# Kernel optimization log

Measured on AMD Instinct MI355X. Metric: run time of the kernel, lower is better.

## Reference

```python
import jax, jax.numpy as jnp
import numpy as np

N_HEADS = 8
N_POINTS = 4


def _grid_sample_bilinear(img, x, y):
    """PyTorch-style grid_sample, mode='bilinear', align_corners=True, zeros padding.
    img: [G, D, Hk, Wk]; x, y: [G, P] pixel coords. Returns [G, D, P]."""
    G, D, Hk, Wk = img.shape
    x0 = jnp.floor(x); y0 = jnp.floor(y)
    x1 = x0 + 1.0; y1 = y0 + 1.0
    wx1 = x - x0; wx0 = 1.0 - wx1
    wy1 = y - y0; wy0 = 1.0 - wy1
    imgf = img.reshape(G, D, Hk * Wk)

    def corner(xi, yi, w):
        valid = (xi >= 0) & (xi <= Wk - 1) & (yi >= 0) & (yi <= Hk - 1)
        ix = jnp.clip(xi, 0, Wk - 1).astype(jnp.int32)
        iy = jnp.clip(yi, 0, Hk - 1).astype(jnp.int32)
        idx = iy * Wk + ix  # [G, P]
        g = jax.vmap(lambda im, i: jnp.take(im, i, axis=1))(imgf, idx)  # [G, D, P]
        return g * (w * valid.astype(w.dtype))[:, None, :]

    return (corner(x0, y0, wx0 * wy0) + corner(x1, y0, wx1 * wy0)
            + corner(x0, y1, wx0 * wy1) + corner(x1, y1, wx1 * wy1))


def setup_inputs() -> dict:
    key = jax.random.key(0)
    ks = jax.random.split(key, 6)
    B, C, H, W = 8, 256, 64, 64
    return {
        "query": jax.random.normal(ks[0], (B, C, H, W), jnp.float32),
        "key": jax.random.normal(ks[1], (B, C, H, W), jnp.float32),
        "w_off": jax.random.normal(ks[2], (N_HEADS * N_POINTS * 3, C), jnp.float32) * 0.02,
        "b_off": jax.random.normal(ks[3], (N_HEADS * N_POINTS * 3,), jnp.float32) * 0.02,
        "w_proj": jax.random.normal(ks[4], (C, C), jnp.float32) * 0.02,
        "b_proj": jax.random.normal(ks[5], (C,), jnp.float32) * 0.02,
    }


def reference(query, key, w_off, b_off, w_proj, b_proj):
    B, C, H, W = query.shape
    Hk, Wk = key.shape[2], key.shape[3]
    d_head = C // N_HEADS

    # [B, N, C]
    q = query.reshape(B, C, H * W).transpose(0, 2, 1)
    ow = q @ w_off.T + b_off                      # [B, N, heads*points*3]
    ow = ow.reshape(B, H, W, N_HEADS, N_POINTS, 3)
    offsets = ow[..., :2]                          # [B,H,W,h,p,2]
    wts = jax.nn.softmax(ow[..., 2], axis=-1)      # [B,H,W,h,p]

    gy, gx = jnp.meshgrid(jnp.linspace(-1.0, 1.0, H, dtype=query.dtype),
                          jnp.linspace(-1.0, 1.0, W, dtype=query.dtype), indexing='ij')
    grid = jnp.stack([gx, gy], axis=-1).reshape(1, H, W, 1, 1, 2)
    locs = grid + offsets * 0.1                    # [B,H,W,h,p,2] normalized coords
    locs = locs.transpose(0, 3, 4, 1, 2, 5)        # [B,h,p,H,W,2]

    G = B * N_HEADS
    locs = locs.reshape(G, N_POINTS * H * W, 2)
    xg = (locs[..., 0] + 1.0) * 0.5 * (Wk - 1)     # align_corners=True mapping
    yg = (locs[..., 1] + 1.0) * 0.5 * (Hk - 1)

    key_r = key.reshape(G, d_head, Hk, Wk)
    sampled = _grid_sample_bilinear(key_r, xg, yg)            # [G, d_head, p*H*W]
    sampled = sampled.reshape(B, N_HEADS, d_head, N_POINTS, H, W)

    w = wts.transpose(0, 3, 4, 1, 2)               # [B,h,p,H,W]
    out_feat = jnp.einsum('bhdpxy,bhpxy->bhdxy', sampled, w)  # [B,h,d,H,W]
    out_feat = out_feat.reshape(B, C, H * W).transpose(0, 2, 1)  # [B,N,C]
    return out_feat @ w_proj.T + b_proj
```

## Files before the change

kernel.cpp:

```cpp
#include <hip/hip_runtime.h>
#include <hip/hip_fp16.h>
#include <cstdint>

#define B_   8
#define C_   256
#define H_   64
#define W_   64
#define HW_  4096
#define NH_  8
#define NP_  4
#define DH_  32

typedef unsigned int u32;
typedef unsigned short u16;
typedef __attribute__((ext_vector_type(8))) short bf16x8;
typedef __attribute__((ext_vector_type(4))) float f32x4;
typedef __attribute__((ext_vector_type(4))) u32 u32x4;
typedef __attribute__((address_space(3))) u32 as3_u32;
typedef __attribute__((address_space(1))) u32 as1_u32;

__device__ __forceinline__ u16 f2bf(float f) {
  u32 u = __builtin_bit_cast(u32, f);
  return (u16)((u + 0x7FFFu + ((u >> 16) & 1u)) >> 16);
}
__device__ __forceinline__ float bflo(u32 v) { return __builtin_bit_cast(float, v << 16); }
__device__ __forceinline__ float bfhi(u32 v) { return __builtin_bit_cast(float, v & 0xFFFF0000u); }

__global__ __launch_bounds__(256) void k_trans_conv(const float* __restrict__ key,
                                                    const float* __restrict__ w_proj,
                                                    u32* __restrict__ key_t2,
                                                    uint2* __restrict__ wproj_bf) {
  __shared__ float tile[32 * 65];
  const int bid = blockIdx.x;
  const int t = threadIdx.x;

  if (bid < 4096) {
    const int g = bid >> 6;
    const int hw0 = (bid & 63) << 6;
    const float* kg = key + (size_t)g * DH_ * HW_ + hw0;
    #pragma unroll
    for (int k = 0; k < 8; ++k) {
      int idx = t + k * 256;
      int d = idx >> 6, j = idx & 63;
      tile[d * 65 + j] = kg[d * HW_ + j];
    }
    __syncthreads();
    u32* kt = key_t2 + ((size_t)g * HW_ + hw0) * 16;
    #pragma unroll
    for (int k = 0; k < 4; ++k) {
      int idx = t + k * 256;
      int j = idx >> 4, dp = idx & 15;
      u32 v = (u32)f2bf(tile[(2 * dp) * 65 + j]) | ((u32)f2bf(tile[(2 * dp + 1) * 65 + j]) << 16);
      kt[j * 16 + dp] = v;
    }
  } else {
    int i = (bid - 4096) * 256 + t;
    float4 v = ((const float4*)w_proj)[i];
    uint2 o;
    o.x = (u32)f2bf(v.x) | ((u32)f2bf(v.y) << 16);
    o.y = (u32)f2bf(v.z) | ((u32)f2bf(v.w) << 16);
    wproj_bf[i] = o;
  }
}

__global__ __launch_bounds__(256) void k_offsets_mfma(const float* __restrict__ query,
                                                      const float* __restrict__ w_off,
                                                      const float* __restrict__ b_off,
                                                      uint2* __restrict__ wpk,
                                                      u32* __restrict__ idx4) {
  __shared__ char smem[81920];
  const int t = threadIdx.x, l = t & 63, w = t >> 6;
  const int lr = l & 15, lq = l >> 4;
  const int r0 = blockIdx.x * 64;
  const int b  = r0 >> 12;
  const int hw0 = r0 & 4095;

  {
    const float4* w4 = (const float4*)w_off;
    #pragma unroll
    for (int j = 0; j < 12; ++j) {
      int m = t + j * 256;
      int col = m >> 5, ch = m & 31;
      float4 lo = w4[m * 2];
      float4 hi = w4[m * 2 + 1];
      u32x4 v;
      v.x = (u32)f2bf(lo.x) | ((u32)f2bf(lo.y) << 16);
      v.y = (u32)f2bf(lo.z) | ((u32)f2bf(lo.w) << 16);
      v.z = (u32)f2bf(hi.x) | ((u32)f2bf(hi.y) << 16);
      v.w = (u32)f2bf(hi.z) | ((u32)f2bf(hi.w) << 16);
      int slot = (col << 5) | (ch ^ (col & 7));
      *(u32x4*)(smem + slot * 16) = v;
    }
  }

  {
    const float* qb = query + ((size_t)b * 256) * 4096 + hw0;
    #pragma unroll
    for (int s = 0; s < 8; ++s) {
      int sid = t + s * 256;
      int kc = sid >> 6, i = sid & 63;
      const float* src = qb + (size_t)(kc * 8) * 4096 + i;
      u32x4 v;
      #pragma unroll
      for (int m = 0; m < 4; ++m) {
        float c0 = src[(size_t)(2 * m) * 4096];
        float c1 = src[(size_t)(2 * m + 1) * 4096];
        ((u32*)&v)[m] = (u32)f2bf(c0) | ((u32)f2bf(c1) << 16);
      }
      *(u32x4*)(smem + 49152 + sid * 16) = v;
    }
  }
  __syncthreads();

  f32x4 acc[6];
  #pragma unroll
  for (int n = 0; n < 6; ++n) acc[n] = (f32x4){0.f, 0.f, 0.f, 0.f};

  #pragma unroll
  for (int step = 0; step < 8; ++step) {
    const int kc = step * 4 + lq;
    bf16x8 af = *(const bf16x8*)(smem + 49152 + (kc * 64 + w * 16 + lr) * 16);
    #pragma unroll
    for (int n = 0; n < 6; ++n) {
      int col = n * 16 + lr;
      bf16x8 bfr = *(const bf16x8*)(smem + ((col << 5) | (kc ^ (col & 7))) * 16);
      acc[n] = __builtin_amdgcn_mfma_f32_16x16x32_bf16(af, bfr, acc[n], 0, 0, 0);
    }
  }
  __syncthreads();

  float* epi = (float*)smem;
  #pragma unroll
  for (int n = 0; n < 6; ++n) {
    int o = n * 16 + lr;
    float bo = b_off[o];
    int row = w * 16 + lq * 4;
    #pragma unroll
    for (int r = 0; r < 4; ++r)
      epi[(row + r) * 98 + o] = acc[n][r] + bo;
  }
  __syncthreads();

  #pragma unroll
  for (int k = 0; k < 2; ++k) {
    int task = t + k * 256;
    int row = task & 63, head = task >> 6;
    const float* o = epi + row * 98 + head * 12;
    float ox[NP_], oy[NP_], lg[NP_];
    #pragma unroll
    for (int p = 0; p < NP_; ++p) {
      ox[p] = o[p * 3 + 0];
      oy[p] = o[p * 3 + 1];
      lg[p] = o[p * 3 + 2];
    }
    float mx = fmaxf(fmaxf(lg[0], lg[1]), fmaxf(lg[2], lg[3]));
    float e[NP_];
    float s = 0.f;
    #pragma unroll
    for (int p = 0; p < NP_; ++p) { e[p] = expf(lg[p] - mx); s += e[p]; }
    float inv = 1.f / s;

    int hw = (r0 + row) & 4095;
    float wq = (float)(hw & 63);
    float hq = (float)(hw >> 6);
    size_t base = ((size_t)(b * NH_ + head) * HW_ + hw) * NP_;
    #pragma unroll
    for (int p = 0; p < NP_; ++p) {
      float wt = e[p] * inv;
      float x = wq + ox[p] * 3.15f;
      float y = hq + oy[p] * 3.15f;
      float x0f = floorf(x), y0f = floorf(y);
      int ix0 = (int)x0f, iy0 = (int)y0f;
      int ix1 = ix0 + 1, iy1 = iy0 + 1;
      float fx = x - x0f, fy = y - y0f;
      float gx0 = 1.f - fx, gy0 = 1.f - fy;

      bool vx0 = (ix0 >= 0) & (ix0 <= W_ - 1);
      bool vx1 = (ix1 >= 0) & (ix1 <= W_ - 1);
      bool vy0 = (iy0 >= 0) & (iy0 <= H_ - 1);
      bool vy1 = (iy1 >= 0) & (iy1 <= H_ - 1);
      int cx0 = min(max(ix0, 0), W_ - 1), cx1 = min(max(ix1, 0), W_ - 1);
      int cy0 = min(max(iy0, 0), H_ - 1), cy1 = min(max(iy1, 0), H_ - 1);

      float w00 = wt * gx0 * gy0 * ((vx0 & vy0) ? 1.f : 0.f);
      float w01 = wt * fx  * gy0 * ((vx1 & vy0) ? 1.f : 0.f);
      float w10 = wt * gx0 * fy  * ((vx0 & vy1) ? 1.f : 0.f);
      float w11 = wt * fx  * fy  * ((vx1 & vy1) ? 1.f : 0.f);

      __half2 h01 = __floats2half2_rn(w00, w01);
      __half2 h23 = __floats2half2_rn(w10, w11);
      uint2 pk;
      pk.x = *(u32*)&h01;
      pk.y = *(u32*)&h23;
      wpk[base + p]  = pk;
      idx4[base + p] = (u32)cx0 | ((u32)cx1 << 6) | ((u32)cy0 << 12) | ((u32)cy1 << 18);
    }
  }
}

__global__ __launch_bounds__(256) void k_sample(const uint2* __restrict__ wpk,
                                                const u32* __restrict__ idx4,
                                                const u32* __restrict__ key_t2,
                                                u32* __restrict__ feat2) {
  const int t = threadIdx.x;
  const int hwid = blockIdx.x * 2 + (t >> 7);
  const int b = hwid >> 12;
  const int hw = hwid & 4095;
  const int c2 = t & 127;
  const int head = c2 >> 4, dp = c2 & 15;
  const int g = b * NH_ + head;
  const size_t pbase = (((size_t)g << 12) + hw) * NP_;
  const u32* kg = key_t2 + ((size_t)g << 16) + dp;

  uint2 Wp[NP_];
  u32 I[NP_];
  #pragma unroll
  for (int p = 0; p < NP_; ++p) { Wp[p] = wpk[pbase + p]; I[p] = idx4[pbase + p]; }

  u32 v00[NP_], v01[NP_], v10[NP_], v11[NP_];
  #pragma unroll
  for (int p = 0; p < NP_; ++p) {
    u32 ip = I[p];
    int cx0 = ip & 63, cx1 = (ip >> 6) & 63, cy0 = (ip >> 12) & 63, cy1 = (ip >> 18) & 63;
    v00[p] = kg[((cy0 << 6) | cx0) * 16];
    v01[p] = kg[((cy0 << 6) | cx1) * 16];
    v10[p] = kg[((cy1 << 6) | cx0) * 16];
    v11[p] = kg[((cy1 << 6) | cx1) * 16];
  }

  float a0 = 0.f, a1 = 0.f;
  #pragma unroll
  for (int p = 0; p < NP_; ++p) {
    float2 w01 = __half22float2(*(const __half2*)&Wp[p].x);
    float2 w23 = __half22float2(*(const __half2*)&Wp[p].y);
    a0 = fmaf(w01.x, bflo(v00[p]), a0);
    a0 = fmaf(w01.y, bflo(v01[p]), a0);
    a0 = fmaf(w23.x, bflo(v10[p]), a0);
    a0 = fmaf(w23.y, bflo(v11[p]), a0);
    a1 = fmaf(w01.x, bfhi(v00[p]), a1);
    a1 = fmaf(w01.y, bfhi(v01[p]), a1);
    a1 = fmaf(w23.x, bfhi(v10[p]), a1);
    a1 = fmaf(w23.y, bfhi(v11[p]), a1);
  }
  feat2[((size_t)b * HW_ + hw) * 128 + c2] = (u32)f2bf(a0) | ((u32)f2bf(a1) << 16);
}

__global__ __launch_bounds__(256) void k_proj_mfma(const u16* __restrict__ A,
                                                   const u16* __restrict__ Bw,
                                                   const float* __restrict__ bias,
                                                   float* __restrict__ out) {
  __shared__ char smem[16384];
  const int t = threadIdx.x, w = t >> 6, l = t & 63;
  const int wm = w >> 1, wn = w & 1;
  const int bid = blockIdx.x;
  const int nb = bid & 1, mb = bid >> 1;
  const int r0 = mb * 128, n0 = nb * 128;

  f32x4 acc[4][4];
  #pragma unroll
  for (int m = 0; m < 4; ++m)
    #pragma unroll
    for (int n = 0; n < 4; ++n)
      acc[m][n] = (f32x4){0.f, 0.f, 0.f, 0.f};

  for (int k0 = 0; k0 < 256; k0 += 32) {
    if (w < 2) {
      #pragma unroll
      for (int j = 0; j < 4; ++j) {
        int i = w * 4 + j;
        int kq = i >> 1, half = i & 1;
        const u16* g = A + ((size_t)(r0 + half * 64 + l)) * 256 + k0 + kq * 8;
        __builtin_amdgcn_global_load_lds((const as1_u32*)g, (as3_u32*)(smem + i * 1024), 16, 0, 0);
      }
    } else {
      #pragma unroll
      for (int j = 0; j < 4; ++j) {
        int i = (w - 2) * 4 + j;
        int kq = i >> 1, half = i & 1;
        const u16* g = Bw + ((size_t)(n0 + half * 64 + l)) * 256 + k0 + kq * 8;
        __builtin_amdgcn_global_load_lds((const as1_u32*)g, (as3_u32*)(smem + 8192 + i * 1024), 16, 0, 0);
      }
    }
    __syncthreads();

    const int kq = l >> 4, lr = l & 15;
    bf16x8 af[4], bfr[4];
    #pragma unroll
    for (int m = 0; m < 4; ++m)
      af[m] = *(const bf16x8*)(smem + (kq * 128 + wm * 64 + m * 16 + lr) * 16);
    #pragma unroll
    for (int n = 0; n < 4; ++n)
      bfr[n] = *(const bf16x8*)(smem + 8192 + (kq * 128 + wn * 64 + n * 16 + lr) * 16);
    #pragma unroll
    for (int m = 0; m < 4; ++m)
      #pragma unroll
      for (int n = 0; n < 4; ++n)
        acc[m][n] = __builtin_amdgcn_mfma_f32_16x16x32_bf16(af[m], bfr[n], acc[m][n], 0, 0, 0);
    __syncthreads();
  }

  const int lr = l & 15, lq = l >> 4;
  #pragma unroll
  for (int n = 0; n < 4; ++n) {
    int col = n0 + wn * 64 + n * 16 + lr;
    float bv = bias[col];
    #pragma unroll
    for (int m = 0; m < 4; ++m) {
      int row = r0 + wm * 64 + m * 16 + lq * 4;
      #pragma unroll
      for (int r = 0; r < 4; ++r)
        out[(size_t)(row + r) * 256 + col] = acc[m][n][r] + bv;
    }
  }
}

extern "C" void kernel_launch(void* const* d_in, const int* in_sizes, int n_in,
                              void* d_out, int out_size, void* d_ws, size_t ws_size,
                              hipStream_t stream) {
  const float* query  = (const float*)d_in[0];
  const float* key    = (const float*)d_in[1];
  const float* w_off  = (const float*)d_in[2];
  const float* b_off  = (const float*)d_in[3];
  const float* w_proj = (const float*)d_in[4];
  const float* b_proj = (const float*)d_in[5];
  float* out = (float*)d_out;

  char* ws = (char*)d_ws;
  uint2*  wpk      = (uint2*)ws;
  u32*    idx4     = (u32*)(ws + (size_t)8  * 1024 * 1024);
  u32*    key_t2   = (u32*)(ws + (size_t)16 * 1024 * 1024);
  u32*    feat2    = (u32*)(ws + (size_t)32 * 1024 * 1024);
  uint2*  wproj_bf = (uint2*)(ws + (size_t)48 * 1024 * 1024);

  hipLaunchKernelGGL(k_trans_conv,   dim3(4160),  dim3(256), 0, stream,
                     key, w_proj, key_t2, wproj_bf);
  hipLaunchKernelGGL(k_offsets_mfma, dim3(512),   dim3(256), 0, stream,
                     query, w_off, b_off, wpk, idx4);
  hipLaunchKernelGGL(k_sample,       dim3(16384), dim3(256), 0, stream,
                     wpk, idx4, key_t2, feat2);
  hipLaunchKernelGGL(k_proj_mfma,    dim3(512),   dim3(256), 0, stream,
                     (const u16*)feat2, (const u16*)wproj_bf, b_proj, out);
}
```

Before: 63.75 us.

## Pre-convert w_off to bf16 once and read MFMA B-fragments from global

The bf16 conversion of w_off moves out of the 512 offset blocks and into 24 extra blocks of the preprocessing kernel. The offsets kernel now reads B fragments directly from global/L2 instead of staging them in LDS, which cuts shared memory from 80KB to 32KB per block and should allow higher occupancy. It also pads the epilogue stride to 97 and switches the wpk/idx4 layout to point-major, so k_sample's per-point loads are coalesced across hw. The cost is more global reads inside the MFMA loop.

New measurement: 81.33 us. 1.28x slower.

```diff
diff --git a/kernel.cpp b/kernel.cpp
--- a/kernel.cpp
+++ b/kernel.cpp
@@ -28,8 +28,10 @@
 
 __global__ __launch_bounds__(256) void k_trans_conv(const float* __restrict__ key,
                                                     const float* __restrict__ w_proj,
+                                                    const float* __restrict__ w_off,
                                                     u32* __restrict__ key_t2,
-                                                    uint2* __restrict__ wproj_bf) {
+                                                    uint2* __restrict__ wproj_bf,
+                                                    u32x4* __restrict__ woff_slots) {
   __shared__ float tile[32 * 65];
   const int bid = blockIdx.x;
   const int t = threadIdx.x;
@@ -53,22 +55,33 @@
       u32 v = (u32)f2bf(tile[(2 * dp) * 65 + j]) | ((u32)f2bf(tile[(2 * dp + 1) * 65 + j]) << 16);
       kt[j * 16 + dp] = v;
     }
-  } else {
+  } else if (bid < 4160) {
     int i = (bid - 4096) * 256 + t;
     float4 v = ((const float4*)w_proj)[i];
     uint2 o;
     o.x = (u32)f2bf(v.x) | ((u32)f2bf(v.y) << 16);
     o.y = (u32)f2bf(v.z) | ((u32)f2bf(v.w) << 16);
     wproj_bf[i] = o;
+  } else {
+    int m = (bid - 4160) * 256 + t;
+    const float4* w4 = (const float4*)w_off;
+    float4 lo = w4[m * 2];
+    float4 hi = w4[m * 2 + 1];
+    u32x4 v;
+    v.x = (u32)f2bf(lo.x) | ((u32)f2bf(lo.y) << 16);
+    v.y = (u32)f2bf(lo.z) | ((u32)f2bf(lo.w) << 16);
+    v.z = (u32)f2bf(hi.x) | ((u32)f2bf(hi.y) << 16);
+    v.w = (u32)f2bf(hi.z) | ((u32)f2bf(hi.w) << 16);
+    woff_slots[m] = v;
   }
 }
 
 __global__ __launch_bounds__(256) void k_offsets_mfma(const float* __restrict__ query,
-                                                      const float* __restrict__ w_off,
+                                                      const u16* __restrict__ woff_slots,
                                                       const float* __restrict__ b_off,
                                                       uint2* __restrict__ wpk,
                                                       u32* __restrict__ idx4) {
-  __shared__ char smem[81920];
+  __shared__ char smem[32768];
   const int t = threadIdx.x, l = t & 63, w = t >> 6;
   const int lr = l & 15, lq = l >> 4;
   const int r0 = blockIdx.x * 64;
@@ -76,24 +89,6 @@
   const int hw0 = r0 & 4095;
 
   {
-    const float4* w4 = (const float4*)w_off;
-    #pragma unroll
-    for (int j = 0; j < 12; ++j) {
-      int m = t + j * 256;
-      int col = m >> 5, ch = m & 31;
-      float4 lo = w4[m * 2];
-      float4 hi = w4[m * 2 + 1];
-      u32x4 v;
-      v.x = (u32)f2bf(lo.x) | ((u32)f2bf(lo.y) << 16);
-      v.y = (u32)f2bf(lo.z) | ((u32)f2bf(lo.w) << 16);
-      v.z = (u32)f2bf(hi.x) | ((u32)f2bf(hi.y) << 16);
-      v.w = (u32)f2bf(hi.z) | ((u32)f2bf(hi.w) << 16);
-      int slot = (col << 5) | (ch ^ (col & 7));
-      *(u32x4*)(smem + slot * 16) = v;
-    }
-  }
-
-  {
     const float* qb = query + ((size_t)b * 256) * 4096 + hw0;
     #pragma unroll
     for (int s = 0; s < 8; ++s) {
@@ -107,7 +102,7 @@
         float c1 = src[(size_t)(2 * m + 1) * 4096];
         ((u32*)&v)[m] = (u32)f2bf(c0) | ((u32)f2bf(c1) << 16);
       }
-      *(u32x4*)(smem + 49152 + sid * 16) = v;
+      *(u32x4*)(smem + sid * 16) = v;
     }
   }
   __syncthreads();
@@ -119,11 +114,11 @@
   #pragma unroll
   for (int step = 0; step < 8; ++step) {
     const int kc = step * 4 + lq;
-    bf16x8 af = *(const bf16x8*)(smem + 49152 + (kc * 64 + w * 16 + lr) * 16);
+    bf16x8 af = *(const bf16x8*)(smem + (kc * 64 + w * 16 + lr) * 16);
     #pragma unroll
     for (int n = 0; n < 6; ++n) {
       int col = n * 16 + lr;
-      bf16x8 bfr = *(const bf16x8*)(smem + ((col << 5) | (kc ^ (col & 7))) * 16);
+      bf16x8 bfr = *(const bf16x8*)(woff_slots + (size_t)(col * 32 + kc) * 8);
       acc[n] = __builtin_amdgcn_mfma_f32_16x16x32_bf16(af, bfr, acc[n], 0, 0, 0);
     }
   }
@@ -137,7 +132,7 @@
     int row = w * 16 + lq * 4;
     #pragma unroll
     for (int r = 0; r < 4; ++r)
-      epi[(row + r) * 98 + o] = acc[n][r] + bo;
+      epi[(row + r) * 97 + o] = acc[n][r] + bo;
   }
   __syncthreads();
 
@@ -145,7 +140,7 @@
   for (int k = 0; k < 2; ++k) {
     int task = t + k * 256;
     int row = task & 63, head = task >> 6;
-    const float* o = epi + row * 98 + head * 12;
+    const float* o = epi + row * 97 + head * 12;
     float ox[NP_], oy[NP_], lg[NP_];
     #pragma unroll
     for (int p = 0; p < NP_; ++p) {
@@ -163,7 +158,7 @@
     int hw = (r0 + row) & 4095;
     float wq = (float)(hw & 63);
     float hq = (float)(hw >> 6);
-    size_t base = ((size_t)(b * NH_ + head) * HW_ + hw) * NP_;
+    int g = b * NH_ + head;
     #pragma unroll
     for (int p = 0; p < NP_; ++p) {
       float wt = e[p] * inv;
@@ -192,8 +187,9 @@
       uint2 pk;
       pk.x = *(u32*)&h01;
       pk.y = *(u32*)&h23;
-      wpk[base + p]  = pk;
-      idx4[base + p] = (u32)cx0 | ((u32)cx1 << 6) | ((u32)cy0 << 12) | ((u32)cy1 << 18);
+      size_t idx = (((size_t)g * NP_ + p) << 12) + hw;
+      wpk[idx]  = pk;
+      idx4[idx] = (u32)cx0 | ((u32)cx1 << 6) | ((u32)cy0 << 12) | ((u32)cy1 << 18);
     }
   }
 }
@@ -209,13 +205,16 @@
   const int c2 = t & 127;
   const int head = c2 >> 4, dp = c2 & 15;
   const int g = b * NH_ + head;
-  const size_t pbase = (((size_t)g << 12) + hw) * NP_;
   const u32* kg = key_t2 + ((size_t)g << 16) + dp;
 
   uint2 Wp[NP_];
   u32 I[NP_];
   #pragma unroll
-  for (int p = 0; p < NP_; ++p) { Wp[p] = wpk[pbase + p]; I[p] = idx4[pbase + p]; }
+  for (int p = 0; p < NP_; ++p) {
+    size_t idx = (((size_t)g * NP_ + p) << 12) + hw;
+    Wp[p] = wpk[idx];
+    I[p]  = idx4[idx];
+  }
 
   u32 v00[NP_], v01[NP_], v10[NP_], v11[NP_];
   #pragma unroll
@@ -331,11 +330,12 @@
   u32*    key_t2   = (u32*)(ws + (size_t)16 * 1024 * 1024);
   u32*    feat2    = (u32*)(ws + (size_t)32 * 1024 * 1024);
   uint2*  wproj_bf = (uint2*)(ws + (size_t)48 * 1024 * 1024);
-
-  hipLaunchKernelGGL(k_trans_conv,   dim3(4160),  dim3(256), 0, stream,
-                     key, w_proj, key_t2, wproj_bf);
+  u32x4*  woff_sl  = (u32x4*)(ws + (size_t)49 * 1024 * 1024);
+
+  hipLaunchKernelGGL(k_trans_conv,   dim3(4184),  dim3(256), 0, stream,
+                     key, w_proj, w_off, key_t2, wproj_bf, woff_sl);
   hipLaunchKernelGGL(k_offsets_mfma, dim3(512),   dim3(256), 0, stream,
-                     query, w_off, b_off, wpk, idx4);
+                     query, (const u16*)woff_sl, b_off, wpk, idx4);
   hipLaunchKernelGGL(k_sample,       dim3(16384), dim3(256), 0, stream,
                      wpk, idx4, key_t2, feat2);
   hipLaunchKernelGGL(k_proj_mfma,    dim3(512),   dim3(256), 0, stream,
```
